# Kernel optimization log

Measured on AMD Instinct MI355X. Metric: run time of the kernel, lower is better.

## Reference

```python
import jax, jax.numpy as jnp
import numpy as np

B = 8192
I = 1024  # input_size
H = 1024  # hidden_size


def setup_inputs() -> dict:
    key = jax.random.key(0)
    ks = jax.random.split(key, 8)
    s_i = 1.0 / np.sqrt(I)
    s_h = 1.0 / np.sqrt(H)
    return {
        "x": jax.random.normal(ks[0], (B, I), dtype=jnp.float32),
        "h": jax.random.normal(ks[1], (B, H), dtype=jnp.float32),
        # nn.Linear weights have shape [out, in]; y = x @ W.T
        "W_wz": jax.random.uniform(ks[2], (H, I), jnp.float32, -s_i, s_i),
        "W_uz": jax.random.uniform(ks[3], (H, H), jnp.float32, -s_h, s_h),
        "W_wr": jax.random.uniform(ks[4], (H, I), jnp.float32, -s_i, s_i),
        "W_ur": jax.random.uniform(ks[5], (H, H), jnp.float32, -s_h, s_h),
        "W_u": jax.random.uniform(ks[6], (H, H), jnp.float32, -s_h, s_h),
        "W_w": jax.random.uniform(ks[7], (H, I), jnp.float32, -s_i, s_i),
    }


def reference(x, h, W_wz, W_uz, W_wr, W_ur, W_u, W_w):
    # Fuse the three x-projections and the two h-projections into grouped GEMMs.
    # [B, 3H] = x @ [I, 3H]
    xp = x @ jnp.concatenate([W_wz, W_wr, W_w], axis=0).T
    hp = h @ jnp.concatenate([W_uz, W_ur], axis=0).T  # [B, 2H]
    z = jax.nn.sigmoid(xp[:, :H] + hp[:, :H])
    r = jax.nn.sigmoid(xp[:, H:2 * H] + hp[:, H:])
    h_t = jnp.tanh((r * h) @ W_u.T + xp[:, 2 * H:])
    return z * h + (1.0 - z) * h_t
```

## Files before the change

### kernel.cpp

```cpp
#include <hip/hip_runtime.h>

typedef unsigned short u16;
typedef __attribute__((ext_vector_type(8))) short bf16x8;
typedef __attribute__((ext_vector_type(4))) float f32x4;

__device__ __forceinline__ u16 f2b(float f) {
  unsigned u = __float_as_uint(f);
  u += 0x7FFFu + ((u >> 16) & 1u);
  return (u16)(u >> 16);
}
__device__ __forceinline__ float sigm(float x) { return 1.0f / (1.0f + __expf(-x)); }
__device__ __forceinline__ float tanh_f(float x) { return 1.0f - 2.0f / (__expf(2.0f * x) + 1.0f); }

__device__ __forceinline__ void cp16(const u16* g, u16* l) {
  __builtin_amdgcn_global_load_lds(
      (const __attribute__((address_space(1))) unsigned int*)g,
      (__attribute__((address_space(3))) unsigned int*)l, 16, 0, 0);
}

__global__ __launch_bounds__(256) void pack_xh(const float* __restrict__ x,
                                               const float* __restrict__ h,
                                               u16* __restrict__ xhb) {
  int idx = blockIdx.x * 256 + threadIdx.x;
  int row = idx >> 9;
  int k = (idx & 511) << 2;
  const float* src = (k < 1024) ? (x + row * 1024 + k) : (h + row * 1024 + (k - 1024));
  float4 v = *reinterpret_cast<const float4*>(src);
  ushort4 o = make_ushort4(f2b(v.x), f2b(v.y), f2b(v.z), f2b(v.w));
  *reinterpret_cast<ushort4*>(xhb + ((size_t)idx << 2)) = o;
}

__global__ __launch_bounds__(256) void pack_w1(const float* __restrict__ Wwz,
                                               const float* __restrict__ Wuz,
                                               const float* __restrict__ Wwr,
                                               const float* __restrict__ Wur,
                                               const float* __restrict__ Ww,
                                               u16* __restrict__ W1b) {
  int idx = blockIdx.x * 256 + threadIdx.x;
  int n = idx >> 9;
  int k = (idx & 511) << 2;
  float4 v = make_float4(0.f, 0.f, 0.f, 0.f);
  if (n < 1024) {
    v = (k < 1024) ? *reinterpret_cast<const float4*>(Wwz + n * 1024 + k)
                   : *reinterpret_cast<const float4*>(Wuz + n * 1024 + (k - 1024));
  } else if (n < 2048) {
    int nn = n - 1024;
    v = (k < 1024) ? *reinterpret_cast<const float4*>(Wwr + nn * 1024 + k)
                   : *reinterpret_cast<const float4*>(Wur + nn * 1024 + (k - 1024));
  } else {
    int nn = n - 2048;
    if (k < 1024) v = *reinterpret_cast<const float4*>(Ww + nn * 1024 + k);
  }
  ushort4 o = make_ushort4(f2b(v.x), f2b(v.y), f2b(v.z), f2b(v.w));
  *reinterpret_cast<ushort4*>(W1b + ((size_t)idx << 2)) = o;
}

__global__ __launch_bounds__(256) void pack_wu(const float* __restrict__ Wu,
                                               u16* __restrict__ Wub) {
  int idx = blockIdx.x * 256 + threadIdx.x;
  float4 v = *reinterpret_cast<const float4*>(Wu + ((size_t)idx << 2));
  ushort4 o = make_ushort4(f2b(v.x), f2b(v.y), f2b(v.z), f2b(v.w));
  *reinterpret_cast<ushort4*>(Wub + ((size_t)idx << 2)) = o;
}

__device__ __forceinline__ void gemm_core(const u16* __restrict__ A, const u16* __restrict__ Bm,
                                          int lda, int ldb, int m0, int n0, int ksteps,
                                          u16* a_lds, u16* b_lds, f32x4 acc[4][4]) {
  const int tid = threadIdx.x;
  const int lane = tid & 63;
  const int wave = tid >> 6;
  const int wr = wave >> 1, wc = wave & 1;
  const int srow = tid >> 2;
  const int scol = (tid & 3) << 3;
  const u16* ga = A + (size_t)(m0 + srow) * lda + scol;
  const u16* gb = Bm + (size_t)(n0 + srow) * ldb + scol;
  u16* la = a_lds + tid * 8;
  u16* lb = b_lds + tid * 8;
  const int fr = lane & 15;
  const int fk = (lane >> 4) << 3;

  for (int kt = 0; kt < ksteps; ++kt) {
    const int k0 = kt * 32;
    cp16(ga + k0, la);
    cp16(ga + (size_t)64 * lda + k0, la + 64 * 32);
    cp16(gb + k0, lb);
    cp16(gb + (size_t)64 * ldb + k0, lb + 64 * 32);
    __syncthreads();

    bf16x8 af[4], bfr[4];
#pragma unroll
    for (int m = 0; m < 4; ++m)
      af[m] = *reinterpret_cast<const bf16x8*>(&a_lds[(wr * 64 + m * 16 + fr) * 32 + fk]);
#pragma unroll
    for (int n = 0; n < 4; ++n)
      bfr[n] = *reinterpret_cast<const bf16x8*>(&b_lds[(wc * 64 + n * 16 + fr) * 32 + fk]);
#pragma unroll
    for (int m = 0; m < 4; ++m)
#pragma unroll
      for (int n = 0; n < 4; ++n)
        acc[m][n] = __builtin_amdgcn_mfma_f32_16x16x32_bf16(af[m], bfr[n], acc[m][n], 0, 0, 0);
    __syncthreads();
  }
}

__global__ __launch_bounds__(256) void gemm1_k(const u16* __restrict__ xhb,
                                               const u16* __restrict__ W1b,
                                               const float* __restrict__ h,
                                               float* __restrict__ zout,
                                               u16* __restrict__ rhb,
                                               float* __restrict__ xwb) {
  __shared__ u16 a_lds[128 * 32];
  __shared__ u16 b_lds[128 * 32];
  const int m0 = blockIdx.y * 128;
  const int n0 = blockIdx.x * 128;
  const int ksteps = (n0 >= 2048) ? 32 : 64;
  f32x4 acc[4][4];
#pragma unroll
  for (int m = 0; m < 4; ++m)
#pragma unroll
    for (int n = 0; n < 4; ++n) acc[m][n] = (f32x4){0.f, 0.f, 0.f, 0.f};

  gemm_core(xhb, W1b, 2048, 2048, m0, n0, ksteps, a_lds, b_lds, acc);

  const int lane = threadIdx.x & 63;
  const int wave = threadIdx.x >> 6;
  const int wr = wave >> 1, wc = wave & 1;
  const int rbase = m0 + wr * 64 + ((lane >> 4) << 2);
  const int cbase = n0 + wc * 64 + (lane & 15);
  const int region = n0 >> 10;
#pragma unroll
  for (int m = 0; m < 4; ++m) {
#pragma unroll
    for (int n = 0; n < 4; ++n) {
      const int col = cbase + n * 16;
#pragma unroll
      for (int j = 0; j < 4; ++j) {
        const int row = rbase + m * 16 + j;
        const float v = acc[m][n][j];
        if (region == 0) {
          zout[(size_t)row * 1024 + col] = sigm(v);
        } else if (region == 1) {
          const size_t idx = (size_t)row * 1024 + (col - 1024);
          rhb[idx] = f2b(sigm(v) * h[idx]);
        } else {
          xwb[(size_t)row * 1024 + (col - 2048)] = v;
        }
      }
    }
  }
}

__global__ __launch_bounds__(256) void gemm2_k(const u16* __restrict__ rhb,
                                               const u16* __restrict__ Wub,
                                               const float* __restrict__ h,
                                               const float* __restrict__ xwb,
                                               float* __restrict__ out) {
  __shared__ u16 a_lds[128 * 32];
  __shared__ u16 b_lds[128 * 32];
  const int m0 = blockIdx.y * 128;
  const int n0 = blockIdx.x * 128;
  f32x4 acc[4][4];
#pragma unroll
  for (int m = 0; m < 4; ++m)
#pragma unroll
    for (int n = 0; n < 4; ++n) acc[m][n] = (f32x4){0.f, 0.f, 0.f, 0.f};

  gemm_core(rhb, Wub, 1024, 1024, m0, n0, 32, a_lds, b_lds, acc);

  const int lane = threadIdx.x & 63;
  const int wave = threadIdx.x >> 6;
  const int wr = wave >> 1, wc = wave & 1;
  const int rbase = m0 + wr * 64 + ((lane >> 4) << 2);
  const int cbase = n0 + wc * 64 + (lane & 15);
#pragma unroll
  for (int m = 0; m < 4; ++m) {
#pragma unroll
    for (int n = 0; n < 4; ++n) {
      const int col = cbase + n * 16;
#pragma unroll
      for (int j = 0; j < 4; ++j) {
        const int row = rbase + m * 16 + j;
        const size_t idx = (size_t)row * 1024 + col;
        const float z = out[idx];
        const float hv = h[idx];
        const float ht = tanh_f(acc[m][n][j] + xwb[idx]);
        out[idx] = z * hv + (1.0f - z) * ht;
      }
    }
  }
}

extern "C" void kernel_launch(void* const* d_in, const int* in_sizes, int n_in,
                              void* d_out, int out_size, void* d_ws, size_t ws_size,
                              hipStream_t stream) {
  const float* x   = (const float*)d_in[0];
  const float* h   = (const float*)d_in[1];
  const float* Wwz = (const float*)d_in[2];
  const float* Wuz = (const float*)d_in[3];
  const float* Wwr = (const float*)d_in[4];
  const float* Wur = (const float*)d_in[5];
  const float* Wu  = (const float*)d_in[6];
  const float* Ww  = (const float*)d_in[7];
  float* out = (float*)d_out;

  char* ws = (char*)d_ws;
  u16*   xhb = (u16*)(ws);
  u16*   W1b = (u16*)(ws + 33554432);
  u16*   Wub = (u16*)(ws + 46137344);
  u16*   rhb = (u16*)(ws + 48234496);
  float* xwb = (float*)(ws + 65011712);

  pack_xh<<<16384, 256, 0, stream>>>(x, h, xhb);
  pack_w1<<<6144, 256, 0, stream>>>(Wwz, Wuz, Wwr, Wur, Ww, W1b);
  pack_wu<<<1024, 256, 0, stream>>>(Wu, Wub);
  gemm1_k<<<dim3(24, 64), 256, 0, stream>>>(xhb, W1b, h, out, rhb, xwb);
  gemm2_k<<<dim3(8, 64), 256, 0, stream>>>(rhb, Wub, h, xwb, out);
}
```

Before: 340.9 us.

## Fuse fp32-to-bf16 conversion into GEMM loads with larger tiles and double buffering

Drops the separate pack kernels. Each GEMM now reads fp32 x, h and weights directly, converts them to bf16 in registers and writes them into swizzled, double-buffered LDS tiles, with the next tile's loads issued before the current MFMAs. Tiles grow to 256x256 or 256x128 with 512 threads, and the W projection moves to its own kernel that writes a bf16 intermediate instead of fp32. This removes the pack passes and their global round trips, but lowers precision of the xw intermediate and gives up async global-to-LDS copies in favour of register staging.

New measurement: 364.0 us. 6.8% more time.

```diff
diff --git a/kernel.cpp b/kernel.cpp
--- a/kernel.cpp
+++ b/kernel.cpp
@@ -2,6 +2,7 @@
 
 typedef unsigned short u16;
 typedef __attribute__((ext_vector_type(8))) short bf16x8;
+typedef __attribute__((ext_vector_type(8))) unsigned short u16x8;
 typedef __attribute__((ext_vector_type(4))) float f32x4;
 
 __device__ __forceinline__ u16 f2b(float f) {
@@ -9,127 +10,117 @@
   u += 0x7FFFu + ((u >> 16) & 1u);
   return (u16)(u >> 16);
 }
+__device__ __forceinline__ float b2f(u16 v) { return __uint_as_float(((unsigned)v) << 16); }
 __device__ __forceinline__ float sigm(float x) { return 1.0f / (1.0f + __expf(-x)); }
 __device__ __forceinline__ float tanh_f(float x) { return 1.0f - 2.0f / (__expf(2.0f * x) + 1.0f); }
 
-__device__ __forceinline__ void cp16(const u16* g, u16* l) {
-  __builtin_amdgcn_global_load_lds(
-      (const __attribute__((address_space(1))) unsigned int*)g,
-      (__attribute__((address_space(3))) unsigned int*)l, 16, 0, 0);
-}
-
-__global__ __launch_bounds__(256) void pack_xh(const float* __restrict__ x,
-                                               const float* __restrict__ h,
-                                               u16* __restrict__ xhb) {
-  int idx = blockIdx.x * 256 + threadIdx.x;
-  int row = idx >> 9;
-  int k = (idx & 511) << 2;
-  const float* src = (k < 1024) ? (x + row * 1024 + k) : (h + row * 1024 + (k - 1024));
-  float4 v = *reinterpret_cast<const float4*>(src);
-  ushort4 o = make_ushort4(f2b(v.x), f2b(v.y), f2b(v.z), f2b(v.w));
-  *reinterpret_cast<ushort4*>(xhb + ((size_t)idx << 2)) = o;
-}
-
-__global__ __launch_bounds__(256) void pack_w1(const float* __restrict__ Wwz,
-                                               const float* __restrict__ Wuz,
-                                               const float* __restrict__ Wwr,
-                                               const float* __restrict__ Wur,
-                                               const float* __restrict__ Ww,
-                                               u16* __restrict__ W1b) {
-  int idx = blockIdx.x * 256 + threadIdx.x;
-  int n = idx >> 9;
-  int k = (idx & 511) << 2;
-  float4 v = make_float4(0.f, 0.f, 0.f, 0.f);
-  if (n < 1024) {
-    v = (k < 1024) ? *reinterpret_cast<const float4*>(Wwz + n * 1024 + k)
-                   : *reinterpret_cast<const float4*>(Wuz + n * 1024 + (k - 1024));
-  } else if (n < 2048) {
-    int nn = n - 1024;
-    v = (k < 1024) ? *reinterpret_cast<const float4*>(Wwr + nn * 1024 + k)
-                   : *reinterpret_cast<const float4*>(Wur + nn * 1024 + (k - 1024));
-  } else {
-    int nn = n - 2048;
-    if (k < 1024) v = *reinterpret_cast<const float4*>(Ww + nn * 1024 + k);
-  }
-  ushort4 o = make_ushort4(f2b(v.x), f2b(v.y), f2b(v.z), f2b(v.w));
-  *reinterpret_cast<ushort4*>(W1b + ((size_t)idx << 2)) = o;
-}
-
-__global__ __launch_bounds__(256) void pack_wu(const float* __restrict__ Wu,
-                                               u16* __restrict__ Wub) {
-  int idx = blockIdx.x * 256 + threadIdx.x;
-  float4 v = *reinterpret_cast<const float4*>(Wu + ((size_t)idx << 2));
-  ushort4 o = make_ushort4(f2b(v.x), f2b(v.y), f2b(v.z), f2b(v.w));
-  *reinterpret_cast<ushort4*>(Wub + ((size_t)idx << 2)) = o;
-}
-
-__device__ __forceinline__ void gemm_core(const u16* __restrict__ A, const u16* __restrict__ Bm,
-                                          int lda, int ldb, int m0, int n0, int ksteps,
-                                          u16* a_lds, u16* b_lds, f32x4 acc[4][4]) {
+__device__ __forceinline__ int swb(int row, int cb) {
+  return row * 64 + (cb ^ ((((row >> 1) & 3)) << 4));
+}
+
+__device__ __forceinline__ void wr8f(u16* dst, float4 a, float4 b) {
+  u16x8 v;
+  v[0] = f2b(a.x); v[1] = f2b(a.y); v[2] = f2b(a.z); v[3] = f2b(a.w);
+  v[4] = f2b(b.x); v[5] = f2b(b.y); v[6] = f2b(b.z); v[7] = f2b(b.w);
+  *reinterpret_cast<u16x8*>(dst) = v;
+}
+
+__global__ __launch_bounds__(512, 2) void gemm_zr(const float* __restrict__ x,
+                                                  const float* __restrict__ h,
+                                                  const float* __restrict__ Wwz,
+                                                  const float* __restrict__ Wuz,
+                                                  const float* __restrict__ Wwr,
+                                                  const float* __restrict__ Wur,
+                                                  float* __restrict__ zout,
+                                                  u16* __restrict__ rhb) {
+  __shared__ u16 A0[8192], A1[8192], B0[8192], B1[8192];
+  const int b = blockIdx.x;
+  const int wg = (b & 7) * 32 + (b >> 3);
+  const int mb = wg >> 3, nb = wg & 7;
+  const int m0 = mb * 256, n0 = nb * 256;
+
   const int tid = threadIdx.x;
   const int lane = tid & 63;
-  const int wave = tid >> 6;
-  const int wr = wave >> 1, wc = wave & 1;
-  const int srow = tid >> 2;
-  const int scol = (tid & 3) << 3;
-  const u16* ga = A + (size_t)(m0 + srow) * lda + scol;
-  const u16* gb = Bm + (size_t)(n0 + srow) * ldb + scol;
-  u16* la = a_lds + tid * 8;
-  u16* lb = b_lds + tid * 8;
-  const int fr = lane & 15;
-  const int fk = (lane >> 4) << 3;
-
-  for (int kt = 0; kt < ksteps; ++kt) {
-    const int k0 = kt * 32;
-    cp16(ga + k0, la);
-    cp16(ga + (size_t)64 * lda + k0, la + 64 * 32);
-    cp16(gb + k0, lb);
-    cp16(gb + (size_t)64 * ldb + k0, lb + 64 * 32);
+  const int wid = tid >> 6;
+  const int wrr = wid >> 2, wcc = wid & 3;
+  const int rS = tid >> 2;
+  const int sS = (tid & 3) * 16;
+  const int kcs = (tid & 3) * 8;
+  const int frow = lane & 15;
+  const int fcb = (lane >> 4) * 16;
+
+  f32x4 acc[8][4];
+#pragma unroll
+  for (int m = 0; m < 8; ++m)
+#pragma unroll
+    for (int n = 0; n < 4; ++n) acc[m][n] = (f32x4){0.f, 0.f, 0.f, 0.f};
+
+  const bool isz = (n0 < 1024);
+
+#define ZR_LOAD(T, a0, a1, a2, a3, b0, b1, b2, b3)                                   \
+  {                                                                                  \
+    const int k1 = (T) * 32;                                                         \
+    const float* Asrc = ((k1 < 1024) ? x : h) + (size_t)(m0 + rS) * 1024 +           \
+                        (k1 & 1023) + kcs;                                           \
+    a0 = *reinterpret_cast<const float4*>(Asrc);                                     \
+    a1 = *reinterpret_cast<const float4*>(Asrc + 4);                                 \
+    a2 = *reinterpret_cast<const float4*>(Asrc + 128 * 1024);                        \
+    a3 = *reinterpret_cast<const float4*>(Asrc + 128 * 1024 + 4);                    \
+    const float* Wz = (k1 < 1024) ? Wwz : Wuz;                                       \
+    const float* Wr = (k1 < 1024) ? Wwr : Wur;                                       \
+    const float* Bb = isz ? (Wz + (size_t)n0 * 1024) : (Wr + (size_t)(n0 - 1024) * 1024); \
+    const float* Bsrc = Bb + (size_t)rS * 1024 + (k1 & 1023) + kcs;                  \
+    b0 = *reinterpret_cast<const float4*>(Bsrc);                                     \
+    b1 = *reinterpret_cast<const float4*>(Bsrc + 4);                                 \
+    b2 = *reinterpret_cast<const float4*>(Bsrc + 128 * 1024);                        \
+    b3 = *reinterpret_cast<const float4*>(Bsrc + 128 * 1024 + 4);                    \
+  }
+
+#define ZR_WRITE(Aw, Bw, a0, a1, a2, a3, b0, b1, b2, b3)                             \
+  {                                                                                  \
+    wr8f((u16*)((char*)Aw + swb(rS, sS)), a0, a1);                                   \
+    wr8f((u16*)((char*)Aw + swb(rS + 128, sS)), a2, a3);                             \
+    wr8f((u16*)((char*)Bw + swb(rS, sS)), b0, b1);                                   \
+    wr8f((u16*)((char*)Bw + swb(rS + 128, sS)), b2, b3);                             \
+  }
+
+#define ZR_TILE(T, Ar, Br, Aw, Bw)                                                   \
+  {                                                                                  \
+    float4 a0, a1, a2, a3, b0, b1, b2, b3;                                           \
+    const bool pf = ((T) + 1 < 64);                                                  \
+    if (pf) ZR_LOAD((T) + 1, a0, a1, a2, a3, b0, b1, b2, b3);                        \
+    bf16x8 af[8];                                                                    \
+    _Pragma("unroll") for (int m = 0; m < 8; ++m)                                    \
+        af[m] = *reinterpret_cast<const bf16x8*>(                                    \
+            (char*)Ar + swb(wrr * 128 + m * 16 + frow, fcb));                        \
+    _Pragma("unroll") for (int n = 0; n < 4; ++n) {                                  \
+      bf16x8 bf = *reinterpret_cast<const bf16x8*>(                                  \
+          (char*)Br + swb(wcc * 64 + n * 16 + frow, fcb));                           \
+      _Pragma("unroll") for (int m = 0; m < 8; ++m)                                  \
+          acc[m][n] = __builtin_amdgcn_mfma_f32_16x16x32_bf16(af[m], bf, acc[m][n], 0, 0, 0); \
+    }                                                                                \
+    if (pf) ZR_WRITE(Aw, Bw, a0, a1, a2, a3, b0, b1, b2, b3);                        \
+    __syncthreads();                                                                 \
+  }
+
+  {
+    float4 a0, a1, a2, a3, b0, b1, b2, b3;
+    ZR_LOAD(0, a0, a1, a2, a3, b0, b1, b2, b3);
+    ZR_WRITE(A0, B0, a0, a1, a2, a3, b0, b1, b2, b3);
     __syncthreads();
-
-    bf16x8 af[4], bfr[4];
-#pragma unroll
-    for (int m = 0; m < 4; ++m)
-      af[m] = *reinterpret_cast<const bf16x8*>(&a_lds[(wr * 64 + m * 16 + fr) * 32 + fk]);
-#pragma unroll
-    for (int n = 0; n < 4; ++n)
-      bfr[n] = *reinterpret_cast<const bf16x8*>(&b_lds[(wc * 64 + n * 16 + fr) * 32 + fk]);
-#pragma unroll
-    for (int m = 0; m < 4; ++m)
-#pragma unroll
-      for (int n = 0; n < 4; ++n)
-        acc[m][n] = __builtin_amdgcn_mfma_f32_16x16x32_bf16(af[m], bfr[n], acc[m][n], 0, 0, 0);
-    __syncthreads();
-  }
-}
-
-__global__ __launch_bounds__(256) void gemm1_k(const u16* __restrict__ xhb,
-                                               const u16* __restrict__ W1b,
-                                               const float* __restrict__ h,
-                                               float* __restrict__ zout,
-                                               u16* __restrict__ rhb,
-                                               float* __restrict__ xwb) {
-  __shared__ u16 a_lds[128 * 32];
-  __shared__ u16 b_lds[128 * 32];
-  const int m0 = blockIdx.y * 128;
-  const int n0 = blockIdx.x * 128;
-  const int ksteps = (n0 >= 2048) ? 32 : 64;
-  f32x4 acc[4][4];
-#pragma unroll
-  for (int m = 0; m < 4; ++m)
-#pragma unroll
-    for (int n = 0; n < 4; ++n) acc[m][n] = (f32x4){0.f, 0.f, 0.f, 0.f};
-
-  gemm_core(xhb, W1b, 2048, 2048, m0, n0, ksteps, a_lds, b_lds, acc);
-
-  const int lane = threadIdx.x & 63;
-  const int wave = threadIdx.x >> 6;
-  const int wr = wave >> 1, wc = wave & 1;
-  const int rbase = m0 + wr * 64 + ((lane >> 4) << 2);
-  const int cbase = n0 + wc * 64 + (lane & 15);
-  const int region = n0 >> 10;
-#pragma unroll
-  for (int m = 0; m < 4; ++m) {
+  }
+  for (int t = 0; t < 64; t += 2) {
+    ZR_TILE(t, A0, B0, A1, B1);
+    ZR_TILE(t + 1, A1, B1, A0, B0);
+  }
+#undef ZR_TILE
+#undef ZR_WRITE
+#undef ZR_LOAD
+
+  const int rbase = m0 + wrr * 128 + ((lane >> 4) << 2);
+  const int cbase = n0 + wcc * 64 + (lane & 15);
+#pragma unroll
+  for (int m = 0; m < 8; ++m) {
 #pragma unroll
     for (int n = 0; n < 4; ++n) {
       const int col = cbase + n * 16;
@@ -137,45 +128,171 @@
       for (int j = 0; j < 4; ++j) {
         const int row = rbase + m * 16 + j;
         const float v = acc[m][n][j];
-        if (region == 0) {
+        if (isz) {
           zout[(size_t)row * 1024 + col] = sigm(v);
-        } else if (region == 1) {
+        } else {
           const size_t idx = (size_t)row * 1024 + (col - 1024);
           rhb[idx] = f2b(sigm(v) * h[idx]);
-        } else {
-          xwb[(size_t)row * 1024 + (col - 2048)] = v;
         }
       }
     }
   }
 }
 
-__global__ __launch_bounds__(256) void gemm2_k(const u16* __restrict__ rhb,
-                                               const u16* __restrict__ Wub,
-                                               const float* __restrict__ h,
-                                               const float* __restrict__ xwb,
-                                               float* __restrict__ out) {
-  __shared__ u16 a_lds[128 * 32];
-  __shared__ u16 b_lds[128 * 32];
-  const int m0 = blockIdx.y * 128;
-  const int n0 = blockIdx.x * 128;
-  f32x4 acc[4][4];
-#pragma unroll
-  for (int m = 0; m < 4; ++m)
-#pragma unroll
-    for (int n = 0; n < 4; ++n) acc[m][n] = (f32x4){0.f, 0.f, 0.f, 0.f};
-
-  gemm_core(rhb, Wub, 1024, 1024, m0, n0, 32, a_lds, b_lds, acc);
-
-  const int lane = threadIdx.x & 63;
-  const int wave = threadIdx.x >> 6;
-  const int wr = wave >> 1, wc = wave & 1;
-  const int rbase = m0 + wr * 64 + ((lane >> 4) << 2);
-  const int cbase = n0 + wc * 64 + (lane & 15);
-#pragma unroll
-  for (int m = 0; m < 4; ++m) {
-#pragma unroll
-    for (int n = 0; n < 4; ++n) {
+#define C2_GEOM()                                   \
+  const int tid = threadIdx.x;                      \
+  const int lane = tid & 63;                        \
+  const int wid = tid >> 6;                         \
+  const int wrr = wid >> 2, wcc = wid & 3;          \
+  const int rS = tid >> 2;                          \
+  const int sS = (tid & 3) * 16;                    \
+  const int kcs = (tid & 3) * 8;                    \
+  const int frow = lane & 15;                       \
+  const int fcb = (lane >> 4) * 16;
+
+#define C2_MFMA(Ar, Br)                                                              \
+  {                                                                                  \
+    bf16x8 af[8];                                                                    \
+    _Pragma("unroll") for (int m = 0; m < 8; ++m)                                    \
+        af[m] = *reinterpret_cast<const bf16x8*>(                                    \
+            (char*)Ar + swb(wrr * 128 + m * 16 + frow, fcb));                        \
+    _Pragma("unroll") for (int n = 0; n < 2; ++n) {                                  \
+      bf16x8 bf = *reinterpret_cast<const bf16x8*>(                                  \
+          (char*)Br + swb(wcc * 32 + n * 16 + frow, fcb));                           \
+      _Pragma("unroll") for (int m = 0; m < 8; ++m)                                  \
+          acc[m][n] = __builtin_amdgcn_mfma_f32_16x16x32_bf16(af[m], bf, acc[m][n], 0, 0, 0); \
+    }                                                                                \
+  }
+
+__global__ __launch_bounds__(512, 2) void gemm_w(const float* __restrict__ x,
+                                                 const float* __restrict__ Ww,
+                                                 u16* __restrict__ xwb) {
+  __shared__ u16 A0[8192], A1[8192], B0[4096], B1[4096];
+  const int b = blockIdx.x;
+  const int wg = (b & 7) * 32 + (b >> 3);
+  const int mb = wg >> 3, nb = wg & 7;
+  const int m0 = mb * 256, n0 = nb * 128;
+  C2_GEOM();
+  f32x4 acc[8][2];
+#pragma unroll
+  for (int m = 0; m < 8; ++m)
+#pragma unroll
+    for (int n = 0; n < 2; ++n) acc[m][n] = (f32x4){0.f, 0.f, 0.f, 0.f};
+
+#define W_LOAD(T, a0, a1, a2, a3, b0, b1)                                            \
+  {                                                                                  \
+    const int k1 = (T) * 32;                                                         \
+    const float* Asrc = x + (size_t)(m0 + rS) * 1024 + k1 + kcs;                     \
+    a0 = *reinterpret_cast<const float4*>(Asrc);                                     \
+    a1 = *reinterpret_cast<const float4*>(Asrc + 4);                                 \
+    a2 = *reinterpret_cast<const float4*>(Asrc + 128 * 1024);                        \
+    a3 = *reinterpret_cast<const float4*>(Asrc + 128 * 1024 + 4);                    \
+    const float* Bsrc = Ww + (size_t)(n0 + rS) * 1024 + k1 + kcs;                    \
+    b0 = *reinterpret_cast<const float4*>(Bsrc);                                     \
+    b1 = *reinterpret_cast<const float4*>(Bsrc + 4);                                 \
+  }
+#define W_WRITE(Aw, Bw, a0, a1, a2, a3, b0, b1)                                      \
+  {                                                                                  \
+    wr8f((u16*)((char*)Aw + swb(rS, sS)), a0, a1);                                   \
+    wr8f((u16*)((char*)Aw + swb(rS + 128, sS)), a2, a3);                             \
+    if (rS < 128) wr8f((u16*)((char*)Bw + swb(rS, sS)), b0, b1);                     \
+  }
+#define W_TILE(T, Ar, Br, Aw, Bw)                                                    \
+  {                                                                                  \
+    float4 a0, a1, a2, a3, b0, b1;                                                   \
+    const bool pf = ((T) + 1 < 32);                                                  \
+    if (pf) W_LOAD((T) + 1, a0, a1, a2, a3, b0, b1);                                 \
+    C2_MFMA(Ar, Br);                                                                 \
+    if (pf) W_WRITE(Aw, Bw, a0, a1, a2, a3, b0, b1);                                 \
+    __syncthreads();                                                                 \
+  }
+  {
+    float4 a0, a1, a2, a3, b0, b1;
+    W_LOAD(0, a0, a1, a2, a3, b0, b1);
+    W_WRITE(A0, B0, a0, a1, a2, a3, b0, b1);
+    __syncthreads();
+  }
+  for (int t = 0; t < 32; t += 2) {
+    W_TILE(t, A0, B0, A1, B1);
+    W_TILE(t + 1, A1, B1, A0, B0);
+  }
+#undef W_TILE
+#undef W_WRITE
+#undef W_LOAD
+
+  const int rbase = m0 + wrr * 128 + ((lane >> 4) << 2);
+  const int cbase = n0 + wcc * 32 + (lane & 15);
+#pragma unroll
+  for (int m = 0; m < 8; ++m)
+#pragma unroll
+    for (int n = 0; n < 2; ++n)
+#pragma unroll
+      for (int j = 0; j < 4; ++j)
+        xwb[(size_t)(rbase + m * 16 + j) * 1024 + cbase + n * 16] = f2b(acc[m][n][j]);
+}
+
+__global__ __launch_bounds__(512, 2) void gemm2_k(const u16* __restrict__ rhb,
+                                                  const float* __restrict__ Wu,
+                                                  const float* __restrict__ h,
+                                                  const u16* __restrict__ xwb,
+                                                  float* __restrict__ out) {
+  __shared__ u16 A0[8192], A1[8192], B0[4096], B1[4096];
+  const int b = blockIdx.x;
+  const int wg = (b & 7) * 32 + (b >> 3);
+  const int mb = wg >> 3, nb = wg & 7;
+  const int m0 = mb * 256, n0 = nb * 128;
+  C2_GEOM();
+  f32x4 acc[8][2];
+#pragma unroll
+  for (int m = 0; m < 8; ++m)
+#pragma unroll
+    for (int n = 0; n < 2; ++n) acc[m][n] = (f32x4){0.f, 0.f, 0.f, 0.f};
+
+#define G2_LOAD(T, a0, a1, b0, b1)                                                   \
+  {                                                                                  \
+    const int k1 = (T) * 32;                                                         \
+    const u16* Asrc = rhb + (size_t)(m0 + rS) * 1024 + k1 + kcs;                     \
+    a0 = *reinterpret_cast<const u16x8*>(Asrc);                                      \
+    a1 = *reinterpret_cast<const u16x8*>(Asrc + 128 * 1024);                         \
+    const float* Bsrc = Wu + (size_t)(n0 + rS) * 1024 + k1 + kcs;                    \
+    b0 = *reinterpret_cast<const float4*>(Bsrc);                                     \
+    b1 = *reinterpret_cast<const float4*>(Bsrc + 4);                                 \
+  }
+#define G2_WRITE(Aw, Bw, a0, a1, b0, b1)                                             \
+  {                                                                                  \
+    *reinterpret_cast<u16x8*>((char*)Aw + swb(rS, sS)) = a0;                         \
+    *reinterpret_cast<u16x8*>((char*)Aw + swb(rS + 128, sS)) = a1;                   \
+    if (rS < 128) wr8f((u16*)((char*)Bw + swb(rS, sS)), b0, b1);                     \
+  }
+#define G2_TILE(T, Ar, Br, Aw, Bw)                                                   \
+  {                                                                                  \
+    u16x8 a0, a1; float4 b0, b1;                                                     \
+    const bool pf = ((T) + 1 < 32);                                                  \
+    if (pf) G2_LOAD((T) + 1, a0, a1, b0, b1);                                        \
+    C2_MFMA(Ar, Br);                                                                 \
+    if (pf) G2_WRITE(Aw, Bw, a0, a1, b0, b1);                                        \
+    __syncthreads();                                                                 \
+  }
+  {
+    u16x8 a0, a1; float4 b0, b1;
+    G2_LOAD(0, a0, a1, b0, b1);
+    G2_WRITE(A0, B0, a0, a1, b0, b1);
+    __syncthreads();
+  }
+  for (int t = 0; t < 32; t += 2) {
+    G2_TILE(t, A0, B0, A1, B1);
+    G2_TILE(t + 1, A1, B1, A0, B0);
+  }
+#undef G2_TILE
+#undef G2_WRITE
+#undef G2_LOAD
+
+  const int rbase = m0 + wrr * 128 + ((lane >> 4) << 2);
+  const int cbase = n0 + wcc * 32 + (lane & 15);
+#pragma unroll
+  for (int m = 0; m < 8; ++m) {
+#pragma unroll
+    for (int n = 0; n < 2; ++n) {
       const int col = cbase + n * 16;
 #pragma unroll
       for (int j = 0; j < 4; ++j) {
@@ -183,7 +300,7 @@
         const size_t idx = (size_t)row * 1024 + col;
         const float z = out[idx];
         const float hv = h[idx];
-        const float ht = tanh_f(acc[m][n][j] + xwb[idx]);
+        const float ht = tanh_f(acc[m][n][j] + b2f(xwb[idx]));
         out[idx] = z * hv + (1.0f - z) * ht;
       }
     }
@@ -204,15 +321,10 @@
   float* out = (float*)d_out;
 
   char* ws = (char*)d_ws;
-  u16*   xhb = (u16*)(ws);
-  u16*   W1b = (u16*)(ws + 33554432);
-  u16*   Wub = (u16*)(ws + 46137344);
-  u16*   rhb = (u16*)(ws + 48234496);
-  float* xwb = (float*)(ws + 65011712);
-
-  pack_xh<<<16384, 256, 0, stream>>>(x, h, xhb);
-  pack_w1<<<6144, 256, 0, stream>>>(Wwz, Wuz, Wwr, Wur, Ww, W1b);
-  pack_wu<<<1024, 256, 0, stream>>>(Wu, Wub);
-  gemm1_k<<<dim3(24, 64), 256, 0, stream>>>(xhb, W1b, h, out, rhb, xwb);
-  gemm2_k<<<dim3(8, 64), 256, 0, stream>>>(rhb, Wub, h, xwb, out);
-}
+  u16* rhb = (u16*)(ws);
+  u16* xwb = (u16*)(ws + 16777216);
+
+  gemm_zr<<<256, 512, 0, stream>>>(x, h, Wwz, Wuz, Wwr, Wur, out, rhb);
+  gemm_w<<<256, 512, 0, stream>>>(x, Ww, xwb);
+  gemm2_k<<<256, 512, 0, stream>>>(rhb, Wu, h, xwb, out);
+}
```
